# Performance work log

Measured on AMD Instinct MI355X. Metric: run time of the kernel, lower is better.

## Reference

```python
import jax, jax.numpy as jnp
import numpy as np

BATCH, CHANNELS, WINDOW, N_PATCHES = 16, 64, 200, 30
D_MODEL = 256
HIDDEN = D_MODEL // 2  # 128


def setup_inputs() -> dict:
    key = jax.random.key(0)
    ks = jax.random.split(key, 7)
    s = 1.0 / np.sqrt(HIDDEN)
    return {
        "x": jax.random.normal(ks[0], (BATCH, CHANNELS, WINDOW, N_PATCHES), dtype=jnp.float32),
        "W_ih": jax.random.normal(ks[1], (4 * HIDDEN, CHANNELS), dtype=jnp.float32) * s,
        "W_hh": jax.random.normal(ks[2], (4 * HIDDEN, HIDDEN), dtype=jnp.float32) * s,
        "b_ih": jax.random.normal(ks[3], (4 * HIDDEN,), dtype=jnp.float32) * s,
        "b_hh": jax.random.normal(ks[4], (4 * HIDDEN,), dtype=jnp.float32) * s,
        "W_fc": jax.random.normal(ks[5], (CHANNELS, HIDDEN), dtype=jnp.float32) * s,
        "b_fc": jax.random.normal(ks[6], (CHANNELS,), dtype=jnp.float32) * s,
    }


def _lstm_last_h(x_seq, W_ih, W_hh, b_ih, b_hh):
    # x_seq: (N, T, C) -> final hidden state (N, H). PyTorch gate order: i, f, g, o.
    N = x_seq.shape[0]
    H = W_hh.shape[1]
    # Precompute input contribution for all timesteps: (N, T, 4H)
    xg = jnp.einsum('ntc,gc->ntg', x_seq, W_ih) + b_ih + b_hh
    xg_t = jnp.swapaxes(xg, 0, 1)  # (T, N, 4H)

    def step(carry, xt):
        h, c = carry
        gates = xt + h @ W_hh.T  # (N, 4H)
        i, f, g, o = jnp.split(gates, 4, axis=-1)
        i = jax.nn.sigmoid(i)
        f = jax.nn.sigmoid(f)
        g = jnp.tanh(g)
        o = jax.nn.sigmoid(o)
        c = f * c + i * g
        h = o * jnp.tanh(c)
        return (h, c), None

    h0 = jnp.zeros((N, H), dtype=x_seq.dtype)
    c0 = jnp.zeros((N, H), dtype=x_seq.dtype)
    (h_T, _), _ = jax.lax.scan(step, (h0, c0), xg_t)
    return h_T


def reference(x, W_ih, W_hh, b_ih, b_hh, W_fc, b_fc):
    batch, channels, window, n_patches = x.shape
    # (B, C, T, P) -> (B, P, T, C) -> (B*P, T, C): each patch is an LSTM sequence
    x_flat = jnp.transpose(x, (0, 3, 2, 1)).reshape(batch * n_patches, window, channels)
    h_last = _lstm_last_h(x_flat, W_ih, W_hh, b_ih, b_hh)  # (B*P, H)
    out = h_last @ W_fc.T + b_fc  # (B*P, C)
    return out.reshape(batch, n_patches, channels)
```

## Files before the change

kernel.cpp:

```cpp
#include <hip/hip_runtime.h>

#define BATCH 16
#define CH    64
#define TLEN  200
#define NP    30
#define HID   128
#define NSEQ  (BATCH * NP)
#define HXP   136
#define XBP   72

typedef _Float16 half8  __attribute__((ext_vector_type(8)));
typedef _Float16 half2v __attribute__((ext_vector_type(2)));
typedef float    f32x4  __attribute__((ext_vector_type(4)));

__device__ __forceinline__ float sigm_fast(float x) {
    return __builtin_amdgcn_rcpf(1.0f + __expf(-x));
}
__device__ __forceinline__ float tanh_fast(float x) {
    float xc = fminf(15.0f, fmaxf(-15.0f, x));
    float e = __expf(2.0f * xc);
    return (e - 1.0f) * __builtin_amdgcn_rcpf(e + 1.0f);
}
__device__ __forceinline__ half8 cvt8(float4 a, float4 b) {
    return (half8){(_Float16)a.x,(_Float16)a.y,(_Float16)a.z,(_Float16)a.w,
                   (_Float16)b.x,(_Float16)b.y,(_Float16)b.z,(_Float16)b.w};
}

#define MFMA16(A,B,C) __builtin_amdgcn_mfma_f32_16x16x32_f16((A),(B),(C),0,0,0)

__global__ __launch_bounds__(512) void fused_lstm(
    const float* __restrict__ x, const float* __restrict__ W_ih,
    const float* __restrict__ W_hh, const float* __restrict__ b_ih,
    const float* __restrict__ b_hh, const float* __restrict__ W_fc,
    const float* __restrict__ b_fc, float* __restrict__ out)
{
    const int tid = threadIdx.x;
    const int w  = tid >> 6;
    const int l  = tid & 63;
    const int lr = l & 15;
    const int lq = l >> 4;

    const int n0 = blockIdx.x * 2;
    const int b0 = n0 / NP;
    const int p0 = n0 % NP;

    __shared__ __align__(16) _Float16 hx2[2][16][HXP];
    __shared__ __align__(16) _Float16 xbuf[2][16][XBP];
    __shared__ __align__(16) _Float16 xgb[2][8][HID][8];

    half8 bhh[4][4];
    half8 bih[4][2];
#pragma unroll
    for (int T = 0; T < 4; ++T) {
        const int g = 128*T + 16*w + lr;
        const float* rh = W_hh + (size_t)g * HID;
        const float* ri = W_ih + (size_t)g * CH;
#pragma unroll
        for (int kt = 0; kt < 4; ++kt) {
            const int k0 = 32*kt + 8*lq;
            bhh[T][kt] = cvt8(*(const float4*)(rh + k0), *(const float4*)(rh + k0 + 4));
        }
#pragma unroll
        for (int j = 0; j < 2; ++j) {
            const int k0 = 32*j + 8*lq;
            bih[T][j] = cvt8(*(const float4*)(ri + k0), *(const float4*)(ri + k0 + 4));
        }
    }
    float bias0, bias1, bias2, bias3;
    {
        const int gb = 16*w + lr;
        bias0 = b_ih[gb]       + b_hh[gb];
        bias1 = b_ih[gb + 128] + b_hh[gb + 128];
        bias2 = b_ih[gb + 256] + b_hh[gb + 256];
        bias3 = b_ih[gb + 384] + b_hh[gb + 384];
    }

    for (int i = tid; i < (2*16*HXP)/2; i += 512) ((unsigned*)hx2)[i] = 0u;

    const bool isload = (l >= 16 && l < 32);
    int ls = 0, lc = 0;
    const float* xbase = nullptr;
    float xpend = 0.f;
    f32x4 xga0, xga1, xga2, xga3;
    half8 xf0, xf1;
    if (isload) {
        const int idx = w * 16 + (l - 16);
        ls = idx >> 6;
        lc = idx & 63;
        xbase = x + ((size_t)(b0 * CH + lc) * TLEN) * NP + p0 + ls;
#pragma unroll
        for (int u = 0; u < 16; ++u)
            xbuf[u >> 3][2*(u & 7) + ls][lc] = (_Float16)xbase[(size_t)u * NP];
        xpend = xbase[(size_t)16 * NP];
    }
    float c0 = 0.f, c1 = 0.f;
    __syncthreads();

#define WRITE_XGA(BUF) {                                                          \
        _Float16* q0_ = &xgb[BUF][2*lq][16*w + lr][0];                            \
        _Float16* q1_ = &xgb[BUF][2*lq + 1][16*w + lr][0];                        \
        *(half2v*)(q0_ + 0) = (half2v){(_Float16)xga0[0], (_Float16)xga1[0]};     \
        *(half2v*)(q0_ + 2) = (half2v){(_Float16)xga2[0], (_Float16)xga3[0]};     \
        *(half2v*)(q0_ + 4) = (half2v){(_Float16)xga0[1], (_Float16)xga1[1]};     \
        *(half2v*)(q0_ + 6) = (half2v){(_Float16)xga2[1], (_Float16)xga3[1]};     \
        *(half2v*)(q1_ + 0) = (half2v){(_Float16)xga0[2], (_Float16)xga1[2]};     \
        *(half2v*)(q1_ + 2) = (half2v){(_Float16)xga2[2], (_Float16)xga3[2]};     \
        *(half2v*)(q1_ + 4) = (half2v){(_Float16)xga0[3], (_Float16)xga1[3]};     \
        *(half2v*)(q1_ + 6) = (half2v){(_Float16)xga2[3], (_Float16)xga3[3]}; }

    {
        const _Float16* xr = &xbuf[0][lr][8 * lq];
        xf0 = *(const half8*)xr;
        xf1 = *(const half8*)(xr + 32);
        xga0 = (f32x4){bias0, bias0, bias0, bias0};
        xga1 = (f32x4){bias1, bias1, bias1, bias1};
        xga2 = (f32x4){bias2, bias2, bias2, bias2};
        xga3 = (f32x4){bias3, bias3, bias3, bias3};
        xga0 = MFMA16(xf0, bih[0][0], xga0); xga0 = MFMA16(xf1, bih[0][1], xga0);
        xga1 = MFMA16(xf0, bih[1][0], xga1); xga1 = MFMA16(xf1, bih[1][1], xga1);
        xga2 = MFMA16(xf0, bih[2][0], xga2); xga2 = MFMA16(xf1, bih[2][1], xga2);
        xga3 = MFMA16(xf0, bih[3][0], xga3); xga3 = MFMA16(xf1, bih[3][1], xga3);
        WRITE_XGA(0)
    }
    __syncthreads();

#define MM4(A, KT)                                                       \
        ci = MFMA16(A, bhh[0][KT], ci); cf = MFMA16(A, bhh[1][KT], cf);  \
        cg = MFMA16(A, bhh[2][KT], cg); co = MFMA16(A, bhh[3][KT], co);

#pragma unroll 1
    for (int p = 0; p < 25; ++p) {
        const int pe = p & 1;
#pragma unroll
        for (int k = 0; k < 8; ++k) {
            const int cur = k & 1;
            const int nxt = cur ^ 1;
            if (k == 0) {
                const _Float16* xr = &xbuf[pe ^ 1][lr][8 * lq];
                xf0 = *(const half8*)xr;
                xf1 = *(const half8*)(xr + 32);
                xga0 = (f32x4){bias0, bias0, bias0, bias0};
                xga1 = (f32x4){bias1, bias1, bias1, bias1};
                xga2 = (f32x4){bias2, bias2, bias2, bias2};
                xga3 = (f32x4){bias3, bias3, bias3, bias3};
            }
            const _Float16* hr = &hx2[cur][lr][8 * lq];
            half8 a0 = *(const half8*)(hr);
            half8 a1 = *(const half8*)(hr + 32);
            half8 a2 = *(const half8*)(hr + 64);
            half8 a3 = *(const half8*)(hr + 96);
            f32x4 ci = {0.f, 0.f, 0.f, 0.f};
            f32x4 cf = ci, cg = ci, co = ci;
            MM4(a0, 0) MM4(a1, 1) MM4(a2, 2) MM4(a3, 3)
            if (k == 0) xga0 = MFMA16(xf0, bih[0][0], xga0);
            if (k == 1) xga0 = MFMA16(xf1, bih[0][1], xga0);
            if (k == 2) xga1 = MFMA16(xf0, bih[1][0], xga1);
            if (k == 3) xga1 = MFMA16(xf1, bih[1][1], xga1);
            if (k == 4) xga2 = MFMA16(xf0, bih[2][0], xga2);
            if (k == 5) xga2 = MFMA16(xf1, bih[2][1], xga2);
            if (k == 6) xga3 = MFMA16(xf0, bih[3][0], xga3);
            if (k == 7) xga3 = MFMA16(xf1, bih[3][1], xga3);

            if (l < 16) {
                half8 xgv = *(const half8*)&xgb[pe][k][16*w + lr][0];
                float gi0 = ci[0] + (float)xgv[0];
                float gf0 = cf[0] + (float)xgv[1];
                float gg0 = cg[0] + (float)xgv[2];
                float go0 = co[0] + (float)xgv[3];
                float gi1 = ci[1] + (float)xgv[4];
                float gf1 = cf[1] + (float)xgv[5];
                float gg1 = cg[1] + (float)xgv[6];
                float go1 = co[1] + (float)xgv[7];
                c0 = sigm_fast(gf0) * c0 + sigm_fast(gi0) * tanh_fast(gg0);
                c1 = sigm_fast(gf1) * c1 + sigm_fast(gi1) * tanh_fast(gg1);
                hx2[nxt][0][16*w + lr] = (_Float16)(sigm_fast(go0) * tanh_fast(c0));
                hx2[nxt][1][16*w + lr] = (_Float16)(sigm_fast(go1) * tanh_fast(c1));
            } else if (l < 32) {
                xbuf[pe][2*k + ls][lc] = (_Float16)xpend;
                int tq = 8*p + k + 17;
                tq = tq > TLEN - 1 ? TLEN - 1 : tq;
                xpend = xbase[(size_t)tq * NP];
            }
            if (k == 7) WRITE_XGA(pe ^ 1)
            __syncthreads();
        }
    }

    if (tid < 2 * CH) {
        const int s = tid >> 6, ch = tid & 63;
        const float* wf = W_fc + (size_t)ch * HID;
        float acc = b_fc[ch];
#pragma unroll
        for (int j8 = 0; j8 < 16; ++j8) {
            half8 hv = *(const half8*)&hx2[0][s][8 * j8];
            float4 w0 = *(const float4*)(wf + 8 * j8);
            float4 w1 = *(const float4*)(wf + 8 * j8 + 4);
            acc += w0.x * (float)hv[0] + w0.y * (float)hv[1]
                 + w0.z * (float)hv[2] + w0.w * (float)hv[3]
                 + w1.x * (float)hv[4] + w1.y * (float)hv[5]
                 + w1.z * (float)hv[6] + w1.w * (float)hv[7];
        }
        out[(size_t)(n0 + s) * CH + ch] = acc;
    }
}

extern "C" void kernel_launch(void* const* d_in, const int* in_sizes, int n_in,
                              void* d_out, int out_size, void* d_ws, size_t ws_size,
                              hipStream_t stream) {
    (void)in_sizes; (void)n_in; (void)out_size; (void)d_ws; (void)ws_size;
    fused_lstm<<<NSEQ / 2, 512, 0, stream>>>(
        (const float*)d_in[0], (const float*)d_in[1], (const float*)d_in[2],
        (const float*)d_in[3], (const float*)d_in[4], (const float*)d_in[5],
        (const float*)d_in[6], (float*)d_out);
}
```

Before: 226.0 us.

## Spread LSTM cell update across 32 lanes and batch input-gate MFMAs

The elementwise LSTM cell update is now spread over 32 lanes, one sequence element each, instead of 16 lanes each handling two. This halves the serial transcendental chain per step. The input projection for the next 8-step block is computed in one burst at k==0, rather than spread one MFMA per step, and is written back with wide half8 stores. Loader lanes move to lanes 32-47. The h value is also written to a duplicate row (s_+4), presumably to fill the MFMA A-operand layout. The cost is more lane work per step and a single heavier step at k==0.

```diff
diff --git a/kernel.cpp b/kernel.cpp
--- a/kernel.cpp
+++ b/kernel.cpp
@@ -10,7 +10,7 @@
 #define XBP   72
 
 typedef _Float16 half8  __attribute__((ext_vector_type(8)));
-typedef _Float16 half2v __attribute__((ext_vector_type(2)));
+typedef _Float16 half4v __attribute__((ext_vector_type(4)));
 typedef float    f32x4  __attribute__((ext_vector_type(4)));
 
 __device__ __forceinline__ float sigm_fast(float x) {
@@ -77,14 +77,12 @@
 
     for (int i = tid; i < (2*16*HXP)/2; i += 512) ((unsigned*)hx2)[i] = 0u;
 
-    const bool isload = (l >= 16 && l < 32);
+    const bool isload = (l >= 32 && l < 48);
     int ls = 0, lc = 0;
     const float* xbase = nullptr;
     float xpend = 0.f;
-    f32x4 xga0, xga1, xga2, xga3;
-    half8 xf0, xf1;
     if (isload) {
-        const int idx = w * 16 + (l - 16);
+        const int idx = w * 16 + (l - 32);
         ls = idx >> 6;
         lc = idx & 63;
         xbase = x + ((size_t)(b0 * CH + lc) * TLEN) * NP + p0 + ls;
@@ -93,35 +91,31 @@
             xbuf[u >> 3][2*(u & 7) + ls][lc] = (_Float16)xbase[(size_t)u * NP];
         xpend = xbase[(size_t)16 * NP];
     }
-    float c0 = 0.f, c1 = 0.f;
+    float cst = 0.f;
+    const int hcol = 16*w + lr;
+    const int sq = lq & 1;
     __syncthreads();
 
-#define WRITE_XGA(BUF) {                                                          \
-        _Float16* q0_ = &xgb[BUF][2*lq][16*w + lr][0];                            \
-        _Float16* q1_ = &xgb[BUF][2*lq + 1][16*w + lr][0];                        \
-        *(half2v*)(q0_ + 0) = (half2v){(_Float16)xga0[0], (_Float16)xga1[0]};     \
-        *(half2v*)(q0_ + 2) = (half2v){(_Float16)xga2[0], (_Float16)xga3[0]};     \
-        *(half2v*)(q0_ + 4) = (half2v){(_Float16)xga0[1], (_Float16)xga1[1]};     \
-        *(half2v*)(q0_ + 6) = (half2v){(_Float16)xga2[1], (_Float16)xga3[1]};     \
-        *(half2v*)(q1_ + 0) = (half2v){(_Float16)xga0[2], (_Float16)xga1[2]};     \
-        *(half2v*)(q1_ + 2) = (half2v){(_Float16)xga2[2], (_Float16)xga3[2]};     \
-        *(half2v*)(q1_ + 4) = (half2v){(_Float16)xga0[3], (_Float16)xga1[3]};     \
-        *(half2v*)(q1_ + 6) = (half2v){(_Float16)xga2[3], (_Float16)xga3[3]}; }
+#define XG_BURST(SB, TB) {                                                        \
+        const _Float16* xr_ = &xbuf[SB][lr][8*lq];                                \
+        half8 xf0_ = *(const half8*)xr_;                                          \
+        half8 xf1_ = *(const half8*)(xr_ + 32);                                   \
+        f32x4 x0_ = {bias0, bias0, bias0, bias0};                                 \
+        f32x4 x1_ = {bias1, bias1, bias1, bias1};                                 \
+        f32x4 x2_ = {bias2, bias2, bias2, bias2};                                 \
+        f32x4 x3_ = {bias3, bias3, bias3, bias3};                                 \
+        x0_ = MFMA16(xf0_, bih[0][0], x0_); x0_ = MFMA16(xf1_, bih[0][1], x0_);   \
+        x1_ = MFMA16(xf0_, bih[1][0], x1_); x1_ = MFMA16(xf1_, bih[1][1], x1_);   \
+        x2_ = MFMA16(xf0_, bih[2][0], x2_); x2_ = MFMA16(xf1_, bih[2][1], x2_);   \
+        x3_ = MFMA16(xf0_, bih[3][0], x3_); x3_ = MFMA16(xf1_, bih[3][1], x3_);   \
+        half8 r0_ = {(_Float16)x0_[0],(_Float16)x1_[0],(_Float16)x2_[0],(_Float16)x3_[0],  \
+                     (_Float16)x0_[1],(_Float16)x1_[1],(_Float16)x2_[1],(_Float16)x3_[1]}; \
+        half8 r1_ = {(_Float16)x0_[2],(_Float16)x1_[2],(_Float16)x2_[2],(_Float16)x3_[2],  \
+                     (_Float16)x0_[3],(_Float16)x1_[3],(_Float16)x2_[3],(_Float16)x3_[3]}; \
+        *(half8*)&xgb[TB][2*lq][hcol][0]     = r0_;                               \
+        *(half8*)&xgb[TB][2*lq + 1][hcol][0] = r1_; }
 
-    {
-        const _Float16* xr = &xbuf[0][lr][8 * lq];
-        xf0 = *(const half8*)xr;
-        xf1 = *(const half8*)(xr + 32);
-        xga0 = (f32x4){bias0, bias0, bias0, bias0};
-        xga1 = (f32x4){bias1, bias1, bias1, bias1};
-        xga2 = (f32x4){bias2, bias2, bias2, bias2};
-        xga3 = (f32x4){bias3, bias3, bias3, bias3};
-        xga0 = MFMA16(xf0, bih[0][0], xga0); xga0 = MFMA16(xf1, bih[0][1], xga0);
-        xga1 = MFMA16(xf0, bih[1][0], xga1); xga1 = MFMA16(xf1, bih[1][1], xga1);
-        xga2 = MFMA16(xf0, bih[2][0], xga2); xga2 = MFMA16(xf1, bih[2][1], xga2);
-        xga3 = MFMA16(xf0, bih[3][0], xga3); xga3 = MFMA16(xf1, bih[3][1], xga3);
-        WRITE_XGA(0)
-    }
+    XG_BURST(0, 0)
     __syncthreads();
 
 #define MM4(A, KT)                                                       \
@@ -135,16 +129,8 @@
         for (int k = 0; k < 8; ++k) {
             const int cur = k & 1;
             const int nxt = cur ^ 1;
-            if (k == 0) {
-                const _Float16* xr = &xbuf[pe ^ 1][lr][8 * lq];
-                xf0 = *(const half8*)xr;
-                xf1 = *(const half8*)(xr + 32);
-                xga0 = (f32x4){bias0, bias0, bias0, bias0};
-                xga1 = (f32x4){bias1, bias1, bias1, bias1};
-                xga2 = (f32x4){bias2, bias2, bias2, bias2};
-                xga3 = (f32x4){bias3, bias3, bias3, bias3};
-            }
-            const _Float16* hr = &hx2[cur][lr][8 * lq];
+            half4v xgv = *(const half4v*)&xgb[pe][k][hcol][4*sq];
+            const _Float16* hr = &hx2[cur][lr][8*lq];
             half8 a0 = *(const half8*)(hr);
             half8 a1 = *(const half8*)(hr + 32);
             half8 a2 = *(const half8*)(hr + 64);
@@ -152,36 +138,25 @@
             f32x4 ci = {0.f, 0.f, 0.f, 0.f};
             f32x4 cf = ci, cg = ci, co = ci;
             MM4(a0, 0) MM4(a1, 1) MM4(a2, 2) MM4(a3, 3)
-            if (k == 0) xga0 = MFMA16(xf0, bih[0][0], xga0);
-            if (k == 1) xga0 = MFMA16(xf1, bih[0][1], xga0);
-            if (k == 2) xga1 = MFMA16(xf0, bih[1][0], xga1);
-            if (k == 3) xga1 = MFMA16(xf1, bih[1][1], xga1);
-            if (k == 4) xga2 = MFMA16(xf0, bih[2][0], xga2);
-            if (k == 5) xga2 = MFMA16(xf1, bih[2][1], xga2);
-            if (k == 6) xga3 = MFMA16(xf0, bih[3][0], xga3);
-            if (k == 7) xga3 = MFMA16(xf1, bih[3][1], xga3);
-
-            if (l < 16) {
-                half8 xgv = *(const half8*)&xgb[pe][k][16*w + lr][0];
-                float gi0 = ci[0] + (float)xgv[0];
-                float gf0 = cf[0] + (float)xgv[1];
-                float gg0 = cg[0] + (float)xgv[2];
-                float go0 = co[0] + (float)xgv[3];
-                float gi1 = ci[1] + (float)xgv[4];
-                float gf1 = cf[1] + (float)xgv[5];
-                float gg1 = cg[1] + (float)xgv[6];
-                float go1 = co[1] + (float)xgv[7];
-                c0 = sigm_fast(gf0) * c0 + sigm_fast(gi0) * tanh_fast(gg0);
-                c1 = sigm_fast(gf1) * c1 + sigm_fast(gi1) * tanh_fast(gg1);
-                hx2[nxt][0][16*w + lr] = (_Float16)(sigm_fast(go0) * tanh_fast(c0));
-                hx2[nxt][1][16*w + lr] = (_Float16)(sigm_fast(go1) * tanh_fast(c1));
-            } else if (l < 32) {
+            if (k == 0 && p < 24) XG_BURST(pe ^ 1, pe ^ 1)
+            if (l < 32) {
+                const bool lo = (l < 16);
+                float gi = (lo ? ci[0] : ci[1]) + (float)xgv[0];
+                float gf = (lo ? cf[0] : cf[1]) + (float)xgv[1];
+                float gg = (lo ? cg[0] : cg[1]) + (float)xgv[2];
+                float go = (lo ? co[0] : co[1]) + (float)xgv[3];
+                cst = sigm_fast(gf) * cst + sigm_fast(gi) * tanh_fast(gg);
+                float hv = sigm_fast(go) * tanh_fast(cst);
+                _Float16 hh = (_Float16)hv;
+                const int s_ = l >> 4;
+                hx2[nxt][s_][hcol]     = hh;
+                hx2[nxt][s_ + 4][hcol] = hh;
+            } else if (isload) {
                 xbuf[pe][2*k + ls][lc] = (_Float16)xpend;
                 int tq = 8*p + k + 17;
                 tq = tq > TLEN - 1 ? TLEN - 1 : tq;
                 xpend = xbase[(size_t)tq * NP];
             }
-            if (k == 7) WRITE_XGA(pe ^ 1)
             __syncthreads();
         }
     }
```

Result: faster. 195.7 us (-13.4%).
